# Kernel tuning notes

Measured on AMD Instinct MI355X. Metric: run time of the kernel, lower is better.

The kernel has to match this reference:

```python
import jax, jax.numpy as jnp
import numpy as np

B, INPUTDIM, OUTDIM, GRIDSIZE = 4096, 128, 512, 300

def setup_inputs() -> dict:
    key = jax.random.key(0)
    k1, k2 = jax.random.split(key)
    x = jax.random.normal(k1, (B, INPUTDIM), dtype=jnp.float32)
    scale = 1.0 / (np.sqrt(INPUTDIM) * np.sqrt(GRIDSIZE))
    fouriercoeffs = jax.random.normal(k2, (2, OUTDIM, INPUTDIM, GRIDSIZE), dtype=jnp.float32) * scale
    return {"x": x, "fouriercoeffs": fouriercoeffs}

def reference(x, fouriercoeffs):
    # k: frequencies 1..gridsize
    gridsize = fouriercoeffs.shape[-1]
    k = jnp.arange(1, gridsize + 1, dtype=x.dtype)  # (G,)
    arg = x[:, :, None] * k  # (B, I, G)
    c = jnp.cos(arg)
    s = jnp.sin(arg)
    # einsum('dbik,djik->bj') with d=2 split into cos/sin terms
    y = jnp.einsum('big,jig->bj', c, fouriercoeffs[0]) + jnp.einsum('big,jig->bj', s, fouriercoeffs[1])
    return y
```

## Files before the change

### kernel.cpp

```cpp
#include <hip/hip_runtime.h>
#include <hip/hip_bf16.h>
#include <cstdint>

#define TB 256

typedef short short8 __attribute__((ext_vector_type(8)));
typedef float f32x4 __attribute__((ext_vector_type(4)));

constexpr int B_N = 4096, I_N = 128, J_N = 512, G_N = 300;
constexpr int K1 = I_N * G_N;
constexpr int BM = 128, BN = 256;
constexpr int NSP = 8;
constexpr int IC = 16;
constexpr float INV2PI = 0.15915494309189535f;

constexpr int GSTRIDE = 4 * 512 * 8;
constexpr size_t SPSTRIDE = (size_t)G_N * GSTRIDE;

__device__ __forceinline__ ushort f2bf(float f) {
    unsigned int u = __float_as_uint(f);
    return (ushort)((u + 0x7FFFu + ((u >> 16) & 1u)) >> 16);
}

__device__ __forceinline__ float fract_(float x) {
#if __has_builtin(__builtin_amdgcn_fractf)
    return __builtin_amdgcn_fractf(x);
#else
    return x - floorf(x);
#endif
}

__device__ __forceinline__ unsigned int pack_bf2(float a, float b) {
    __hip_bfloat162 h = __float22bfloat162_rn(make_float2(a, b));
    unsigned int u;
    __builtin_memcpy(&u, &h, 4);
    return u;
}

typedef __attribute__((address_space(3))) unsigned int lds_u32_t;
typedef __attribute__((address_space(1))) const unsigned int glb_u32_t;

__device__ __forceinline__ void llds16(const void* g, void* l) {
    __builtin_amdgcn_global_load_lds(
        reinterpret_cast<glb_u32_t*>(reinterpret_cast<uintptr_t>(g)),
        reinterpret_cast<lds_u32_t*>((unsigned int)reinterpret_cast<uintptr_t>(l)),
        16, 0, 0);
}

constexpr int TRG = 60;
constexpr int TRTB = 512;
constexpr int TRUNITS = 256 * 15;

__global__ __launch_bounds__(TRTB) void fkan_tr(const float* __restrict__ src,
                                                ushort* __restrict__ dst) {
    __shared__ __align__(16) ushort L[TRG * 2 * 32 * 8];
    const int gc = blockIdx.x;
    const int sp = blockIdx.y;
    const int djc = blockIdx.z;
    const int dj0 = djc * 32;
    const int d = dj0 >> 9;
    const int j0 = dj0 & 511;
    const int g0 = gc * TRG;
    const int tid = threadIdx.x;

    unsigned int* Lw = (unsigned int*)L;

    for (int u = tid; u < TRUNITS; u += TRTB) {
        int rp = u / 15, c = u - rp * 15;
        int djl = rp >> 3, ilp = rp & 7;
        int ihl = ilp >> 2, e2 = ilp & 3;
        const float* p = src + ((size_t)(dj0 + djl) * 128 + sp * 16 + ilp * 2) * 300
                       + g0 + c * 4;
        float4 va = *(const float4*)p;
        float4 vb = *(const float4*)(p + 300);
        float a[4] = {va.x, va.y, va.z, va.w};
        float b[4] = {vb.x, vb.y, vb.z, vb.w};
        const int swz = (c & 7) << 2;
#pragma unroll
        for (int k = 0; k < 4; ++k) {
            int gl = c * 4 + k;
            int wd = ((gl * 2 + ihl) * 32 + djl) * 4 + e2;
            Lw[wd ^ swz] = pack_bf2(a[k], b[k]);
        }
    }
    __syncthreads();

    const uint4* Lv = (const uint4*)L;
    for (int w = tid; w < TRG * 64; w += TRTB) {
        int gl = w >> 6, r = w & 63;
        int ihl = r >> 5, jl = r & 31;
        int q = (gl * 64 + ihl * 32 + jl) ^ ((gl >> 2) & 7);
        size_t d16 = ((size_t)(sp * G_N + g0 + gl) * 4 + d * 2 + ihl) * 512 + j0 + jl;
        ((uint4*)dst)[d16] = Lv[q];
    }
}

__global__ __launch_bounds__(TB, 2)
void fkan_gemm(const float* __restrict__ x,
               const ushort* __restrict__ fcb,
               float* __restrict__ out) {
    __shared__ __align__(16) ushort At[2 * 4 * 128 * 8];
    __shared__ __align__(16) ushort Bt[2 * 4 * 256 * 8];

    const int tid = threadIdx.x;
    const int bm = blockIdx.x, bn = blockIdx.y, sp = blockIdx.z;
    const int lane = tid & 63, wid = tid >> 6;
    const int wm = wid & 1, wn = wid >> 1;
    const int lhi = lane >> 4, llo = lane & 15;
    const int m = tid & 127, half = tid >> 7;

    float sv[8], cv[8], s0[8], c0[8];
    {
        const float* xr = x + ((size_t)(bm * BM + m)) * I_N + sp * IC + half * 8;
        float4 xa = *(const float4*)xr;
        float4 xb = *(const float4*)(xr + 4);
        float xv[8] = {xa.x, xa.y, xa.z, xa.w, xb.x, xb.y, xb.z, xb.w};
#pragma unroll
        for (int j = 0; j < 8; ++j) {
            float r = fract_(xv[j] * INV2PI);
            s0[j] = __builtin_amdgcn_sinf(r);
            c0[j] = __builtin_amdgcn_cosf(r);
            sv[j] = s0[j];
            cv[j] = c0[j];
        }
    }

    const ushort* bp[4];
#pragma unroll
    for (int q = 0; q < 4; ++q)
        bp[q] = fcb + (size_t)sp * SPSTRIDE
              + ((size_t)wid * 512 + bn * BN + q * 64 + lane) * 8;

    const int aoff = (lhi * 128 + wm * 64 + llo) * 8;
    const int boff = (lhi * 256 + wn * 128 + llo) * 8;
    ushort* awc0 = &At[(half * 128 + m) * 8];
    ushort* aws0 = &At[((2 + half) * 128 + m) * 8];

    f32x4 acc[4][8];
#pragma unroll
    for (int a = 0; a < 4; ++a)
#pragma unroll
        for (int b = 0; b < 8; ++b) acc[a][b] = (f32x4){0.f, 0.f, 0.f, 0.f};

    auto stageB = [&](int nb) {
#pragma unroll
        for (int q = 0; q < 4; ++q) {
            llds16(bp[q], (char*)Bt + (size_t)(nb * 1024 + wid * 256 + q * 64) * 16);
            bp[q] += GSTRIDE;
        }
    };
    auto writeA = [&](int nb) {
        uint4 vc = {pack_bf2(cv[0], cv[1]), pack_bf2(cv[2], cv[3]),
                    pack_bf2(cv[4], cv[5]), pack_bf2(cv[6], cv[7])};
        *(uint4*)(awc0 + nb * 4096) = vc;
        uint4 vs = {pack_bf2(sv[0], sv[1]), pack_bf2(sv[2], sv[3]),
                    pack_bf2(sv[4], sv[5]), pack_bf2(sv[6], sv[7])};
        *(uint4*)(aws0 + nb * 4096) = vs;
#pragma unroll
        for (int j = 0; j < 8; ++j) {
            float t = __builtin_fmaf(sv[j], c0[j], cv[j] * s0[j]);
            cv[j] = __builtin_fmaf(cv[j], c0[j], -(sv[j] * s0[j]));
            sv[j] = t;
        }
    };
    auto halfstep = [&](int cb, bool doNext) {
        __syncthreads();
        short8 af[4], bfr[8];
#pragma unroll
        for (int t = 0; t < 4; ++t)
            af[t] = *(const short8*)&At[cb * 4096 + aoff + t * 128];
#pragma unroll
        for (int t = 0; t < 8; ++t)
            bfr[t] = *(const short8*)&Bt[cb * 8192 + boff + t * 128];
        if (doNext) stageB(cb ^ 1);
#pragma unroll
        for (int tm = 0; tm < 4; ++tm)
#pragma unroll
            for (int tn = 0; tn < 8; ++tn)
                acc[tm][tn] = __builtin_amdgcn_mfma_f32_16x16x32_bf16(
                    af[tm], bfr[tn], acc[tm][tn], 0, 0, 0);
        if (doNext) writeA(cb ^ 1);
    };

    writeA(0);
    stageB(0);

    for (int g = 0; g < G_N; g += 2) {
        halfstep(0, true);
        halfstep(1, g + 2 < G_N);
    }

    const int row0 = bm * BM + wm * 64 + lhi * 4;
    const int col0 = bn * BN + wn * 128 + llo;
#pragma unroll
    for (int tm = 0; tm < 4; ++tm)
#pragma unroll
        for (int tn = 0; tn < 8; ++tn)
#pragma unroll
            for (int r = 0; r < 4; ++r)
                atomicAdd(&out[(size_t)(row0 + tm * 16 + r) * J_N + col0 + tn * 16],
                          acc[tm][tn][r]);
}

constexpr int SPL_FB = 4;
constexpr int KS_FB = 2 * K1 / SPL_FB;
constexpr int NSTEP_FB = KS_FB / 32;

__global__ __launch_bounds__(TB)
void fkan_gemm_fb(const float* __restrict__ x,
                  const float* __restrict__ fc32,
                  float* __restrict__ out) {
    __shared__ float xs[BM][65];
    __shared__ __align__(16) ushort At[4 * 128 * 8];
    __shared__ __align__(16) ushort Bt[4 * 128 * 8];

    const int tid = threadIdx.x;
    const int bm = blockIdx.x, bn = blockIdx.y, sp = blockIdx.z;
    const int d = sp >> 1;
    const int ib = (sp & 1) << 6;
    const int rbase = ib * G_N;

    for (int idx = tid; idx < BM * 64; idx += TB) {
        int row = idx >> 6, il = idx & 63;
        xs[row][il] = x[(size_t)(bm * BM + row) * I_N + ib + il];
    }

    f32x4 acc[4][4];
#pragma unroll
    for (int a = 0; a < 4; ++a)
#pragma unroll
        for (int b = 0; b < 4; ++b) acc[a][b] = (f32x4){0.f, 0.f, 0.f, 0.f};

    const int lane = tid & 63, wid = tid >> 6;
    const int wm = wid & 1, wn = wid >> 1;
    const int lhi = lane >> 4, llo = lane & 15;
    const int am = tid & 127, akg0 = tid >> 7;

    const float* f32base = fc32 + ((size_t)d * J_N + bn * 128) * K1 + rbase;

    for (int step = 0; step < NSTEP_FB; ++step) {
        __syncthreads();
#pragma unroll
        for (int it = 0; it < 2; ++it) {
            const int kg = akg0 + it * 2;
            int r = rbase + step * 32 + kg * 8;
            int i = (int)((unsigned)r / 300u);
            int g = r - i * 300;
            float xxv = xs[am][i - ib];
            float kkf = (float)(g + 1);
            short8 avv;
#pragma unroll
            for (int j = 0; j < 8; ++j) {
                float rev = xxv * kkf * INV2PI;
                float fr = fract_(rev) + (d ? 0.0f : 0.25f);
                avv[j] = (short)f2bf(__builtin_amdgcn_sinf(fract_(fr)));
                if (j < 7) {
                    ++g; kkf += 1.0f;
                    if (g == 300) { g = 0; kkf = 1.0f; ++i; xxv = xs[am][i - ib]; }
                }
            }
            *(short8*)&At[(kg * 128 + am) * 8] = avv;
        }
#pragma unroll
        for (int it = 0; it < 2; ++it) {
            int item = tid + it * TB;
            int n = item >> 2, grp = item & 3;
            const float* gp = f32base + (size_t)n * K1 + step * 32 + grp * 8;
            float4 v0 = *(const float4*)gp;
            float4 v1 = *(const float4*)(gp + 4);
            short8 bv;
            bv[0] = (short)f2bf(v0.x); bv[1] = (short)f2bf(v0.y);
            bv[2] = (short)f2bf(v0.z); bv[3] = (short)f2bf(v0.w);
            bv[4] = (short)f2bf(v1.x); bv[5] = (short)f2bf(v1.y);
            bv[6] = (short)f2bf(v1.z); bv[7] = (short)f2bf(v1.w);
            *(short8*)&Bt[(grp * 128 + n) * 8] = bv;
        }
        __syncthreads();
        short8 af[4], bf[4];
#pragma unroll
        for (int t = 0; t < 4; ++t) {
            af[t] = *(const short8*)&At[(lhi * 128 + wm * 64 + t * 16 + llo) * 8];
            bf[t] = *(const short8*)&Bt[(lhi * 128 + wn * 64 + t * 16 + llo) * 8];
        }
#pragma unroll
        for (int tm = 0; tm < 4; ++tm)
#pragma unroll
            for (int tn = 0; tn < 4; ++tn)
                acc[tm][tn] = __builtin_amdgcn_mfma_f32_16x16x32_bf16(
                    af[tm], bf[tn], acc[tm][tn], 0, 0, 0);
    }

    const int row0 = bm * BM + wm * 64 + lhi * 4;
    const int col0 = bn * 128 + wn * 64 + llo;
#pragma unroll
    for (int tm = 0; tm < 4; ++tm)
#pragma unroll
        for (int tn = 0; tn < 4; ++tn)
#pragma unroll
            for (int r = 0; r < 4; ++r)
                atomicAdd(&out[(size_t)(row0 + tm * 16 + r) * J_N + col0 + tn * 16],
                          acc[tm][tn][r]);
}

extern "C" void kernel_launch(void* const* d_in, const int* in_sizes, int n_in,
                              void* d_out, int out_size, void* d_ws, size_t ws_size,
                              hipStream_t stream) {
    const float* x = (const float*)d_in[0];
    const float* fc = (const float*)d_in[1];
    float* out = (float*)d_out;

    hipMemsetAsync(d_out, 0, (size_t)out_size * sizeof(float), stream);

    const size_t need = (size_t)2 * J_N * K1 * sizeof(ushort);

    if (ws_size >= need) {
        ushort* fcb = (ushort*)d_ws;
        fkan_tr<<<dim3(5, 8, 32), TRTB, 0, stream>>>(fc, fcb);
        dim3 grid(B_N / BM, J_N / BN, NSP);
        fkan_gemm<<<grid, TB, 0, stream>>>(x, fcb, out);
    } else {
        dim3 grid(B_N / BM, J_N / 128, SPL_FB);
        fkan_gemm_fb<<<grid, TB, 0, stream>>>(x, fc, out);
    }
}
```

Before: 535.2 us.

## Triple-buffer GEMM LDS stages with explicit waitcnt barriers and MFMA priority

Moves the main GEMM loop from double to triple buffering of the A and B LDS tiles. B tiles are now prefetched two steps ahead, with an explicit s_waitcnt vmcnt(4) replacing a full drain before each raw s_barrier. The MFMA block is bracketed with s_setprio, and the transpose kernel's loops are manually unrolled. The aim is to hide global-to-LDS load latency behind more compute. In exchange it uses more LDS, which may hurt occupancy, and the hand-coded vmcnt value has to match the number of outstanding loads issued per stage.

```diff
diff --git a/kernel.cpp b/kernel.cpp
--- a/kernel.cpp
+++ b/kernel.cpp
@@ -65,7 +65,7 @@
 
     unsigned int* Lw = (unsigned int*)L;
 
-    for (int u = tid; u < TRUNITS; u += TRTB) {
+    auto rbody = [&](int u) {
         int rp = u / 15, c = u - rp * 15;
         int djl = rp >> 3, ilp = rp & 7;
         int ihl = ilp >> 2, e2 = ilp & 3;
@@ -82,25 +82,31 @@
             int wd = ((gl * 2 + ihl) * 32 + djl) * 4 + e2;
             Lw[wd ^ swz] = pack_bf2(a[k], b[k]);
         }
-    }
+    };
+#pragma unroll
+    for (int it = 0; it < 7; ++it) rbody(tid + it * TRTB);
+    if (tid < TRUNITS - 7 * TRTB) rbody(tid + 7 * TRTB);
     __syncthreads();
 
     const uint4* Lv = (const uint4*)L;
-    for (int w = tid; w < TRG * 64; w += TRTB) {
+    auto wbody = [&](int w) {
         int gl = w >> 6, r = w & 63;
         int ihl = r >> 5, jl = r & 31;
         int q = (gl * 64 + ihl * 32 + jl) ^ ((gl >> 2) & 7);
         size_t d16 = ((size_t)(sp * G_N + g0 + gl) * 4 + d * 2 + ihl) * 512 + j0 + jl;
         ((uint4*)dst)[d16] = Lv[q];
-    }
+    };
+#pragma unroll
+    for (int it = 0; it < 7; ++it) wbody(tid + it * TRTB);
+    if (tid < TRG * 64 - 7 * TRTB) wbody(tid + 7 * TRTB);
 }
 
 __global__ __launch_bounds__(TB, 2)
 void fkan_gemm(const float* __restrict__ x,
                const ushort* __restrict__ fcb,
                float* __restrict__ out) {
-    __shared__ __align__(16) ushort At[2 * 4 * 128 * 8];
-    __shared__ __align__(16) ushort Bt[2 * 4 * 256 * 8];
+    __shared__ __align__(16) ushort At[3 * 4 * 128 * 8];
+    __shared__ __align__(16) ushort Bt[3 * 4 * 256 * 8];
 
     const int tid = threadIdx.x;
     const int bm = blockIdx.x, bn = blockIdx.y, sp = blockIdx.z;
@@ -163,8 +169,15 @@
             sv[j] = t;
         }
     };
-    auto halfstep = [&](int cb, bool doNext) {
-        __syncthreads();
+
+    for (int a = 0; a < 1; ++a) {}
+    auto gstep = [&](int g, int cb, bool doNext) {
+        if (g < G_N - 2)
+            asm volatile("s_waitcnt lgkmcnt(0) vmcnt(4)" ::: "memory");
+        else
+            asm volatile("s_waitcnt lgkmcnt(0) vmcnt(0)" ::: "memory");
+        __builtin_amdgcn_s_barrier();
+        __builtin_amdgcn_sched_barrier(0);
         short8 af[4], bfr[8];
 #pragma unroll
         for (int t = 0; t < 4; ++t)
@@ -172,22 +185,28 @@
 #pragma unroll
         for (int t = 0; t < 8; ++t)
             bfr[t] = *(const short8*)&Bt[cb * 8192 + boff + t * 128];
-        if (doNext) stageB(cb ^ 1);
+        const int nb = (cb >= 1) ? (cb - 1) : 2;
+        if (doNext) stageB(nb);
+        __builtin_amdgcn_s_setprio(1);
 #pragma unroll
         for (int tm = 0; tm < 4; ++tm)
 #pragma unroll
             for (int tn = 0; tn < 8; ++tn)
                 acc[tm][tn] = __builtin_amdgcn_mfma_f32_16x16x32_bf16(
                     af[tm], bfr[tn], acc[tm][tn], 0, 0, 0);
-        if (doNext) writeA(cb ^ 1);
+        __builtin_amdgcn_s_setprio(0);
+        if (doNext) writeA(nb);
     };
 
     writeA(0);
     stageB(0);
-
-    for (int g = 0; g < G_N; g += 2) {
-        halfstep(0, true);
-        halfstep(1, g + 2 < G_N);
+    writeA(1);
+    stageB(1);
+
+    for (int g = 0; g < G_N; g += 3) {
+        gstep(g + 0, 0, g + 2 < G_N);
+        gstep(g + 1, 1, g + 3 < G_N);
+        gstep(g + 2, 2, g + 4 < G_N);
     }
 
     const int row0 = bm * BM + wm * 64 + lhi * 4;
```

Result: slower. 914.8 us (+70.9%).
